# Kernel optimization log

Measured on AMD Instinct MI355X. Metric: run time of the kernel, lower is better.

Reference implementation:

```python
import jax, jax.numpy as jnp
import numpy as np

B, NQ, HW, D, H = 4, 100, 4096, 1024, 16
HD = D // H  # head dim = 64
EPS = 1e-5
NEG = -1e9


def layernorm(x, g, b):
    mu = jnp.mean(x, axis=-1, keepdims=True)
    var = jnp.mean(jnp.square(x - mu), axis=-1, keepdims=True)
    return (x - mu) * jax.lax.rsqrt(var + EPS) * g + b


def setup_inputs() -> dict:
    key = jax.random.key(0)
    ks = jax.random.split(key, 6)
    scale = 0.02
    return {
        "q": jax.random.normal(ks[0], (B, NQ, D), dtype=jnp.float32),
        "kv": jax.random.normal(ks[1], (B, HW, D), dtype=jnp.float32),
        "mask": jax.random.randint(ks[2], (B, NQ, HW), 0, 2, dtype=jnp.int32),
        "in_proj_w": scale * jax.random.normal(ks[3], (3 * D, D), dtype=jnp.float32),
        "in_proj_b": jnp.zeros((3 * D,), dtype=jnp.float32),
        "out_w": scale * jax.random.normal(ks[4], (D, D), dtype=jnp.float32),
        "out_b": jnp.zeros((D,), dtype=jnp.float32),
        "g_q": jnp.ones((D,), dtype=jnp.float32),
        "b_q": jnp.zeros((D,), dtype=jnp.float32),
        "g_kv": jnp.ones((D,), dtype=jnp.float32),
        "b_kv": jnp.zeros((D,), dtype=jnp.float32),
    }


def reference(q, kv, mask, in_proj_w, in_proj_b, out_w, out_b, g_q, b_q, g_kv, b_kv):
    qn = layernorm(q, g_q, b_q)      # [B,NQ,D]
    kvn = layernorm(kv, g_kv, b_kv)  # [B,HW,D]

    # nn.MultiheadAttention fused in-projection: rows [Wq; Wk; Wv]
    Wq, Wk, Wv = jnp.split(in_proj_w, 3, axis=0)
    bq, bk, bv = jnp.split(in_proj_b, 3, axis=0)
    qp = (qn @ Wq.T + bq).reshape(B, NQ, H, HD)
    kp = (kvn @ Wk.T + bk).reshape(B, HW, H, HD)
    vp = (kvn @ Wv.T + bv).reshape(B, HW, H, HD)

    scores = jnp.einsum("bqhd,bkhd->bhqk", qp, kp) / jnp.sqrt(jnp.float32(HD))

    # Per-query key mask; a query with an all-zero mask attends everywhere
    # (original code sets key_padding_mask=None when kpm.all()).
    allowed = mask.astype(bool)                                   # [B,NQ,HW]
    has_any = jnp.any(allowed, axis=-1, keepdims=True)
    eff = jnp.where(has_any, allowed, True)
    scores = jnp.where(eff[:, None, :, :], scores, NEG)

    attn = jax.nn.softmax(scores, axis=-1)                        # [B,H,NQ,HW]
    ctx = jnp.einsum("bhqk,bkhd->bqhd", attn, vp).reshape(B, NQ, D)
    return ctx @ out_w.T + out_b
```

## Files before the change

kernel.cpp:

```cpp
#include <hip/hip_runtime.h>
#include <math.h>
#include <stdint.h>

#define B_    4
#define NQ_   100
#define HW_   4096
#define D_    1024
#define H_    16
#define HD_   64
#define NCH_  8
#define KCH_  (HW_/NCH_)
#define QT_   32
#define MP_   512

typedef __attribute__((ext_vector_type(8))) short short8;
typedef __attribute__((ext_vector_type(8))) unsigned short ushort8v;
typedef __attribute__((ext_vector_type(4))) float f32x4;

__device__ __forceinline__ unsigned short f2bf(float f) {
    unsigned int u = __float_as_uint(f);
    u += 0x7fffu + ((u >> 16) & 1u);
    return (unsigned short)(u >> 16);
}
__device__ __forceinline__ float bf2f(unsigned short h) {
    return __uint_as_float(((unsigned int)h) << 16);
}

__device__ __forceinline__ void gl2lds16(const void* g, void* l) {
    typedef __attribute__((address_space(1))) unsigned int gu32;
    typedef __attribute__((address_space(3))) unsigned int lu32;
    __builtin_amdgcn_global_load_lds(
        reinterpret_cast<gu32*>(reinterpret_cast<uintptr_t>(g)),
        reinterpret_cast<lu32*>(reinterpret_cast<uintptr_t>(l)),
        16, 0, 0);
}

#define VMCNT3() asm volatile("s_waitcnt vmcnt(3)" ::: "memory")
#define VMCNT0() asm volatile("s_waitcnt vmcnt(0)" ::: "memory")
#define BARRIER() do { __builtin_amdgcn_s_barrier(); \
                       __builtin_amdgcn_sched_barrier(0); } while (0)

__global__ __launch_bounds__(256) void ln_bf16_kernel(
    const float* __restrict__ x, const float* __restrict__ g,
    const float* __restrict__ be, unsigned short* __restrict__ y, int real_rows)
{
    const int wv = threadIdx.x >> 6, lane = threadIdx.x & 63;
    const int row = blockIdx.x * 4 + wv;
    unsigned short* yr = y + (size_t)row * D_;
    if (row >= real_rows) {
        #pragma unroll
        for (int k = 0; k < 4; ++k)
            *reinterpret_cast<ushort4*>(yr + lane*4 + k*256) = make_ushort4(0,0,0,0);
        return;
    }
    const float* xr = x + (size_t)row * D_;
    float4 v[4];
    float s = 0.f, ss = 0.f;
    #pragma unroll
    for (int k = 0; k < 4; ++k) {
        v[k] = *reinterpret_cast<const float4*>(xr + lane*4 + k*256);
        s  += v[k].x + v[k].y + v[k].z + v[k].w;
        ss += v[k].x*v[k].x + v[k].y*v[k].y + v[k].z*v[k].z + v[k].w*v[k].w;
    }
    #pragma unroll
    for (int o = 1; o < 64; o <<= 1) {
        s  += __shfl_xor(s,  o);
        ss += __shfl_xor(ss, o);
    }
    const float mu = s * (1.0f / D_);
    const float rs = rsqrtf(ss * (1.0f / D_) - mu*mu + 1e-5f);
    #pragma unroll
    for (int k = 0; k < 4; ++k) {
        const float4 gg = *reinterpret_cast<const float4*>(g  + lane*4 + k*256);
        const float4 bb = *reinterpret_cast<const float4*>(be + lane*4 + k*256);
        ushort4 o;
        o.x = f2bf((v[k].x - mu) * rs * gg.x + bb.x);
        o.y = f2bf((v[k].y - mu) * rs * gg.y + bb.y);
        o.z = f2bf((v[k].z - mu) * rs * gg.z + bb.z);
        o.w = f2bf((v[k].w - mu) * rs * gg.w + bb.w);
        *reinterpret_cast<ushort4*>(yr + lane*4 + k*256) = o;
    }
}

__global__ __launch_bounds__(256) void wconv_kernel(
    const float* __restrict__ w, unsigned short* __restrict__ wb)
{
    const int i = blockIdx.x * 256 + threadIdx.x;
    const float4 v = reinterpret_cast<const float4*>(w)[i];
    ushort4 o;
    o.x = f2bf(v.x); o.y = f2bf(v.y); o.z = f2bf(v.z); o.w = f2bf(v.w);
    reinterpret_cast<ushort4*>(wb)[i] = o;
}

__global__ __launch_bounds__(256) void hilo_a_kernel(
    const float* __restrict__ x, unsigned short* __restrict__ y)
{
    const int row = blockIdx.x;
    const int tid = threadIdx.x;
    unsigned short* yr = y + (size_t)row * 3072;
    if (row >= B_*NQ_) {
        const ushort4 z = make_ushort4(0,0,0,0);
        reinterpret_cast<ushort4*>(yr)[tid]        = z;
        reinterpret_cast<ushort4*>(yr + 1024)[tid] = z;
        reinterpret_cast<ushort4*>(yr + 2048)[tid] = z;
        return;
    }
    const float4 v = reinterpret_cast<const float4*>(x + (size_t)row * D_)[tid];
    ushort4 hi, lo;
    hi.x = f2bf(v.x); hi.y = f2bf(v.y); hi.z = f2bf(v.z); hi.w = f2bf(v.w);
    lo.x = f2bf(v.x - bf2f(hi.x)); lo.y = f2bf(v.y - bf2f(hi.y));
    lo.z = f2bf(v.z - bf2f(hi.z)); lo.w = f2bf(v.w - bf2f(hi.w));
    reinterpret_cast<ushort4*>(yr)[tid]        = hi;
    reinterpret_cast<ushort4*>(yr + 1024)[tid] = lo;
    reinterpret_cast<ushort4*>(yr + 2048)[tid] = hi;
}

__global__ __launch_bounds__(256) void hilo_w_kernel(
    const float* __restrict__ w, unsigned short* __restrict__ y)
{
    const int row = blockIdx.x;
    const int tid = threadIdx.x;
    const float4 v = reinterpret_cast<const float4*>(w + (size_t)row * D_)[tid];
    ushort4 hi, lo;
    hi.x = f2bf(v.x); hi.y = f2bf(v.y); hi.z = f2bf(v.z); hi.w = f2bf(v.w);
    lo.x = f2bf(v.x - bf2f(hi.x)); lo.y = f2bf(v.y - bf2f(hi.y));
    lo.z = f2bf(v.z - bf2f(hi.z)); lo.w = f2bf(v.w - bf2f(hi.w));
    unsigned short* yr = y + (size_t)row * 3072;
    reinterpret_cast<ushort4*>(yr)[tid]        = hi;
    reinterpret_cast<ushort4*>(yr + 1024)[tid] = hi;
    reinterpret_cast<ushort4*>(yr + 2048)[tid] = lo;
}

__global__ __launch_bounds__(256) void mpack_kernel(
    const int* __restrict__ mask, unsigned int* __restrict__ mp)
{
    const int qrow = blockIdx.x;
    const int b = blockIdx.y;
    const int tid = threadIdx.x;
    unsigned int word = 0;
    if (qrow < NQ_ && tid < 128) {
        const int4* mr = reinterpret_cast<const int4*>(
            mask + ((size_t)(b*NQ_ + qrow))*HW_ + tid*32);
        #pragma unroll
        for (int j = 0; j < 8; ++j) {
            const int4 v = mr[j];
            word |= (v.x!=0 ? 1u:0u) << (4*j);
            word |= (v.y!=0 ? 1u:0u) << (4*j+1);
            word |= (v.z!=0 ? 1u:0u) << (4*j+2);
            word |= (v.w!=0 ? 1u:0u) << (4*j+3);
        }
    }
    const int wany = __any(word != 0) ? 1 : 0;
    __shared__ int red[4];
    if ((tid & 63) == 0) red[tid >> 6] = wany;
    __syncthreads();
    const int hasany = red[0] | red[1] | red[2] | red[3];
    if (tid < 128)
        mp[((size_t)(b*128 + qrow))*128 + tid] = hasany ? word : 0xFFFFFFFFu;
}

__global__ __launch_bounds__(512, 4) void gemm_kv_kernel(
    const unsigned short* __restrict__ A, const unsigned short* __restrict__ Wb,
    const float* __restrict__ bias, unsigned short* __restrict__ kp,
    unsigned short* __restrict__ vt)
{
    extern __shared__ __align__(16) unsigned short lds[];

    const int tid  = threadIdx.x;
    const int wave = tid >> 6;
    const int lane = tid & 63;
    const int lr   = lane & 15, quad = lane >> 4;
    const int wm2  = wave >> 2;
    const int wn4  = wave & 3;

    const int bn = blockIdx.x & 15;
    const int bm = blockIdx.x >> 4;

    const int srow = tid >> 2;
    const int sswz = (srow & 3) ^ ((srow >> 2) & 3);
    const int scol = ((tid & 3) ^ sswz) * 8;
    const unsigned short* aSrc0 = A  + (size_t)(bm*256 + srow      )*D_ + scol;
    const unsigned short* aSrc1 = A  + (size_t)(bm*256 + srow + 128)*D_ + scol;
    const unsigned short* bSrc  = Wb + (size_t)(bn*128 + srow      )*D_ + scol;
    const int wdst = wave * 512;

    int aoff[8], boff[2];
    #pragma unroll
    for (int fm = 0; fm < 8; ++fm) {
        const int row = wm2*128 + fm*16 + lr;
        aoff[fm] = row*32 + (quad ^ (row & 3) ^ ((row >> 2) & 3))*8;
    }
    #pragma unroll
    for (int fn = 0; fn < 2; ++fn) {
        const int row = wn4*32 + fn*16 + lr;
        boff[fn] = 8192 + row*32 + (quad ^ (row & 3) ^ ((row >> 2) & 3))*8;
    }

    f32x4 acc[8][2];
    #pragma unroll
    for (int i = 0; i < 8; ++i)
        #pragma unroll
        for (int j = 0; j < 2; ++j)
            acc[i][j] = (f32x4){0.f, 0.f, 0.f, 0.f};

    #pragma unroll
    for (int pt = 0; pt < 2; ++pt) {
        gl2lds16(aSrc0 + pt*32, lds + pt*12288 +        wdst);
        gl2lds16(aSrc1 + pt*32, lds + pt*12288 + 4096 + wdst);
        gl2lds16(bSrc  + pt*32, lds + pt*12288 + 8192 + wdst);
    }
    aSrc0 += 64; aSrc1 += 64; bSrc += 64;
    VMCNT3();
    BARRIER();

    int cur = 0, nx2 = 2;
    #pragma unroll 1
    for (int t = 0; t < 32; ++t) {
        const unsigned short* Sl = lds + cur*12288;
        unsigned short*       S2 = lds + nx2*12288;
        short8 afr[4], bfr[2];

        #pragma unroll
        for (int fm = 0; fm < 4; ++fm)
            afr[fm] = *reinterpret_cast<const short8*>(&Sl[aoff[fm]]);
        bfr[0] = *reinterpret_cast<const short8*>(&Sl[boff[0]]);
        bfr[1] = *reinterpret_cast<const short8*>(&Sl[boff[1]]);
        if (t < 30) {
            gl2lds16(aSrc0, S2 +        wdst);
            gl2lds16(aSrc1, S2 + 4096 + wdst);
        }
        __builtin_amdgcn_s_setprio(1);
        #pragma unroll
        for (int fm = 0; fm < 4; ++fm)
            #pragma unroll
            for (int fn = 0; fn < 2; ++fn)
                acc[fm][fn] = __builtin_amdgcn_mfma_f32_16x16x32_bf16(
                    afr[fm], bfr[fn], acc[fm][fn], 0, 0, 0);
        __builtin_amdgcn_s_setprio(0);

        #pragma unroll
        for (int fm = 0; fm < 4; ++fm)
            afr[fm] = *reinterpret_cast<const short8*>(&Sl[aoff[fm + 4]]);
        if (t < 30) {
            gl2lds16(bSrc, S2 + 8192 + wdst);
            aSrc0 += 32; aSrc1 += 32; bSrc += 32;
        }
        __builtin_amdgcn_s_setprio(1);
        #pragma unroll
        for (int fm = 0; fm < 4; ++fm)
            #pragma unroll
            for (int fn = 0; fn < 2; ++fn)
                acc[fm + 4][fn] = __builtin_amdgcn_mfma_f32_16x16x32_bf16(
                    afr[fm], bfr[fn], acc[fm + 4][fn], 0, 0, 0);
        __builtin_amdgcn_s_setprio(0);

        if (t < 30)       { VMCNT3(); }
        else if (t == 30) { VMCNT0(); }
        BARRIER();
        cur = (cur == 2) ? 0 : cur + 1;
        nx2 = (nx2 == 2) ? 0 : nx2 + 1;
    }

    const int colbase = bn*128 + wn4*32 + lr;
    const int mbase   = bm*256 + wm2*128 + quad*4;
    if (bn < 8) {
        #pragma unroll
        for (int fn = 0; fn < 2; ++fn) {
            const int n = colbase + fn*16;
            const float bb = bias[n];
            #pragma unroll
            for (int fm = 0; fm < 8; ++fm) {
                unsigned short* Cp = kp + (size_t)(mbase + fm*16)*1024 + n;
                #pragma unroll
                for (int r = 0; r < 4; ++r)
                    Cp[(size_t)r * 1024] = f2bf(acc[fm][fn][r] + bb);
            }
        }
    } else {
        const int b = bm >> 4;
        const int key0 = mbase - b*4096;
        #pragma unroll
        for (int fn = 0; fn < 2; ++fn) {
            const int n = colbase + fn*16;
            const float bb = bias[n];
            unsigned short* vrow = vt + (size_t)(b*1024 + n - 1024) * HW_;
            #pragma unroll
            for (int fm = 0; fm < 8; ++fm) {
                ushort4 o;
                o.x = f2bf(acc[fm][fn][0] + bb);
                o.y = f2bf(acc[fm][fn][1] + bb);
                o.z = f2bf(acc[fm][fn][2] + bb);
                o.w = f2bf(acc[fm][fn][3] + bb);
                *reinterpret_cast<ushort4*>(vrow + key0 + fm*16) = o;
            }
        }
    }
}

__global__ __launch_bounds__(256) void gemm_splitk_kernel(
    const unsigned short* __restrict__ A, const unsigned short* __restrict__ W,
    float* __restrict__ P, int K, int KS)
{
    __shared__ __align__(16) unsigned short As[2048];
    __shared__ __align__(16) unsigned short Bs[2048];
    const int tid = threadIdx.x;
    const int wave = tid >> 6, lane = tid & 63;
    const int lr = lane & 15, quad = lane >> 4;
    const int bn = blockIdx.x, bm = blockIdx.y, sk = blockIdx.z;

    const int r0 = tid >> 2;
    const int xs = (r0 & 3) ^ ((r0 >> 2) & 3);
    const int kc = (tid & 3) ^ xs;
    const unsigned short* ap = A + (size_t)(bm*64 + r0)*K + sk*KS + kc*8;
    const unsigned short* bp = W + (size_t)(bn*64 + r0)*K + sk*KS + kc*8;
    unsigned short* asd = As + wave*512;
    unsigned short* bsd = Bs + wave*512;

    f32x4 acc[4];
    #pragma unroll
    for (int j = 0; j < 4; ++j) acc[j] = (f32x4){0.f,0.f,0.f,0.f};

    const int arow = wave*16 + lr;
    const int xa = (arow & 3) ^ ((arow >> 2) & 3);
    const int aoff = (arow*4 + (quad ^ xa))*8;
    int boff[4];
    #pragma unroll
    for (int j = 0; j < 4; ++j) {
        const int brow = j*16 + lr;
        const int xb = (brow & 3) ^ ((brow >> 2) & 3);
        boff[j] = (brow*4 + (quad ^ xb))*8;
    }

    const int nsteps = KS >> 5;
    for (int s = 0; s < nsteps; ++s) {
        gl2lds16(ap, asd); gl2lds16(bp, bsd);
        ap += 32; bp += 32;
        __syncthreads();
        const short8 af = *reinterpret_cast<const short8*>(&As[aoff]);
        short8 bf[4];
        #pragma unroll
        for (int j = 0; j < 4; ++j)
            bf[j] = *reinterpret_cast<const short8*>(&Bs[boff[j]]);
        #pragma unroll
        for (int j = 0; j < 4; ++j)
            acc[j] = __builtin_amdgcn_mfma_f32_16x16x32_bf16(af, bf[j], acc[j], 0, 0, 0);
        __syncthreads();
    }

    float* Pb = P + ((size_t)sk*MP_ + bm*64)*1024 + bn*64;
    const int m0 = wave*16 + quad*4;
    #pragma unroll
    for (int j = 0; j < 4; ++j)
        #pragma unroll
        for (int r = 0; r < 4; ++r)
            Pb[(size_t)(m0 + r)*1024 + j*16 + lr] = acc[j][r];
}

__global__ __launch_bounds__(256) void reduce_kernel(
    const float* __restrict__ P, const float* __restrict__ bias,
    float* __restrict__ Cout, int SK)
{
    const int i4 = blockIdx.x * 256 + threadIdx.x;
    const int c4 = i4 & 255;
    float4 s = reinterpret_cast<const float4*>(bias)[c4];
    for (int sk = 0; sk < SK; ++sk) {
        const float4 p = reinterpret_cast<const float4*>(P + (size_t)sk*MP_*1024)[i4];
        s.x += p.x; s.y += p.y; s.z += p.z; s.w += p.w;
    }
    reinterpret_cast<float4*>(Cout)[i4] = s;
}

__global__ __launch_bounds__(256) void flash_kernel(
    const float* __restrict__ qp, const unsigned short* __restrict__ kp,
    const unsigned short* __restrict__ vt, const unsigned int* __restrict__ mpack,
    float* __restrict__ partO, float* __restrict__ partL)
{
    __shared__ __align__(16) unsigned char smem[49152];
    unsigned short* Ks  = (unsigned short*)smem;
    unsigned short* Vts = (unsigned short*)(smem + 16384);
    unsigned short* Qs  = (unsigned short*)(smem + 32768);
    unsigned short* Ps  = (unsigned short*)(smem + 37376);
    unsigned int*   MWs = (unsigned int*)  (smem + 47616);
    float*          mlW = (float*)         (smem + 48128);
    float*          Om  = (float*)smem;

    const int tid = threadIdx.x;
    const int wave = tid >> 6, lane = tid & 63;
    const int lr = lane & 15, quad = lane >> 4;
    const int qt = blockIdx.x, h = blockIdx.y;
    const int b = blockIdx.z >> 3, ks = blockIdx.z & 7;
    const int kb0 = ks * KCH_;

    {
        const int q = tid >> 3, dc = (tid & 7) * 8;
        const int qg = qt*QT_ + q;
        float4 v0 = make_float4(0.f,0.f,0.f,0.f), v1 = v0;
        if (qg < NQ_) {
            const float* src = qp + ((size_t)(b*NQ_ + qg))*D_ + h*HD_ + dc;
            v0 = *reinterpret_cast<const float4*>(src);
            v1 = *reinterpret_cast<const float4*>(src + 4);
        }
        ushort8v o;
        o[0]=f2bf(v0.x*0.125f); o[1]=f2bf(v0.y*0.125f);
        o[2]=f2bf(v0.z*0.125f); o[3]=f2bf(v0.w*0.125f);
        o[4]=f2bf(v1.x*0.125f); o[5]=f2bf(v1.y*0.125f);
        o[6]=f2bf(v1.z*0.125f); o[7]=f2bf(v1.w*0.125f);
        *reinterpret_cast<ushort8v*>(&Qs[q*72 + dc]) = o;
    }

    const unsigned short* kptr[4];
    const unsigned short* vptr[4];
    #pragma unroll
    for (int i = 0; i < 4; ++i) {
        const int s = i*256 + tid;
        const int key = s >> 3, jg = (s & 7) ^ (key & 7);
        kptr[i] = kp + ((size_t)(b*HW_) + kb0 + key)*1024 + h*HD_ + jg*8;
        const int d = s >> 4, js = s & 15, jg2 = js ^ (d & 15);
        vptr[i] = vt + ((size_t)(b*1024 + h*HD_ + d))*HW_ + kb0 + jg2*8;
    }

    int koff[2][2], voff[4];
    #pragma unroll
    for (int kj = 0; kj < 2; ++kj)
        #pragma unroll
        for (int ds = 0; ds < 2; ++ds) {
            const int key_l = wave*32 + kj*16 + lr;
            const int jg = ds*4 + quad;
            koff[kj][ds] = (key_l*8 + (jg ^ (key_l & 7))) * 8;
        }
    #pragma unroll
    for (int dj = 0; dj < 4; ++dj) {
        const int d_l = dj*16 + lr;
        const int jg = wave*4 + quad;
        voff[dj] = (d_l*16 + (jg ^ (d_l & 15))) * 8;
    }

    float lreg[8];
    #pragma unroll
    for (int i = 0; i < 8; ++i) lreg[i] = 0.f;
    f32x4 Ov[2][4];
    #pragma unroll
    for (int i = 0; i < 2; ++i)
        #pragma unroll
        for (int j = 0; j < 4; ++j)
            Ov[i][j] = (f32x4){0.f,0.f,0.f,0.f};

    for (int kt = 0; kt < 4; ++kt) {
        __syncthreads();
        #pragma unroll
        for (int i = 0; i < 4; ++i) {
            gl2lds16(kptr[i], Ks  + (i*256 + wave*64)*8);
            gl2lds16(vptr[i], Vts + (i*256 + wave*64)*8);
            kptr[i] += 128*1024; vptr[i] += 128;
        }
        if (tid < 128) {
            const int mw = tid >> 5, mq = tid & 31;
            MWs[mw*32 + mq] = mpack[((size_t)(b*128 + qt*QT_ + mq))*128 +
                                    (ks*16 + kt*4 + mw)];
        }
        __syncthreads();

        f32x4 S[2][2];
        #pragma unroll
        for (int i = 0; i < 2; ++i)
            #pragma unroll
            for (int kj = 0; kj < 2; ++kj)
                S[i][kj] = (f32x4){0.f,0.f,0.f,0.f};
        #pragma unroll
        for (int ds = 0; ds < 2; ++ds) {
            short8 aq[2], bk[2];
            aq[0] = *reinterpret_cast<const short8*>(&Qs[(     lr)*72 + ds*32 + quad*8]);
            aq[1] = *reinterpret_cast<const short8*>(&Qs[(16 + lr)*72 + ds*32 + quad*8]);
            bk[0] = *reinterpret_cast<const short8*>(&Ks[koff[0][ds]]);
            bk[1] = *reinterpret_cast<const short8*>(&Ks[koff[1][ds]]);
            #pragma unroll
            for (int i = 0; i < 2; ++i)
                #pragma unroll
                for (int kj = 0; kj < 2; ++kj)
                    S[i][kj] = __builtin_amdgcn_mfma_f32_16x16x32_bf16(
                        aq[i], bk[kj], S[i][kj], 0, 0, 0);
        }

        #pragma unroll
        for (int i = 0; i < 2; ++i) {
            #pragma unroll
            for (int r = 0; r < 4; ++r) {
                const int q = i*16 + quad*4 + r;
                const unsigned int mw = MWs[wave*32 + q];
                const float p0 = ((mw >> lr) & 1u)        ? __expf(S[i][0][r]) : 0.f;
                const float p1 = ((mw >> (16 + lr)) & 1u) ? __expf(S[i][1][r]) : 0.f;
                lreg[i*4+r] += p0 + p1;
                const float p0n = __shfl_xor(p0, 1);
                const float p1n = __shfl_xor(p1, 1);
                if (!(lr & 1)) {
                    const unsigned int w0 = (unsigned)f2bf(p0) | ((unsigned)f2bf(p0n) << 16);
                    const unsigned int w1 = (unsigned)f2bf(p1) | ((unsigned)f2bf(p1n) << 16);
                    *reinterpret_cast<unsigned int*>(&Ps[wave*1280 + q*40 + lr])      = w0;
                    *reinterpret_cast<unsigned int*>(&Ps[wave*1280 + q*40 + 16 + lr]) = w1;
                }
            }
        }

        short8 pf[2], vf[4];
        #pragma unroll
        for (int i = 0; i < 2; ++i)
            pf[i] = *reinterpret_cast<const short8*>(&Ps[wave*1280 + (i*16+lr)*40 + quad*8]);
        #pragma unroll
        for (int dj = 0; dj < 4; ++dj)
            vf[dj] = *reinterpret_cast<const short8*>(&Vts[voff[dj]]);
        #pragma unroll
        for (int i = 0; i < 2; ++i)
            #pragma unroll
            for (int dj = 0; dj < 4; ++dj)
                Ov[i][dj] = __builtin_amdgcn_mfma_f32_16x16x32_bf16(
                    pf[i], vf[dj], Ov[i][dj], 0, 0, 0);
    }

    __syncthreads();
    #pragma unroll
    for (int i = 0; i < 2; ++i)
        #pragma unroll
        for (int r = 0; r < 4; ++r) {
            float l = lreg[i*4+r];
            #pragma unroll
            for (int o = 1; o < 16; o <<= 1) l += __shfl_xor(l, o);
            if (lr == 0) mlW[wave*32 + i*16 + quad*4 + r] = l;
        }
    #pragma unroll
    for (int i = 0; i < 2; ++i)
        #pragma unroll
        for (int dj = 0; dj < 4; ++dj)
            #pragma unroll
            for (int r = 0; r < 4; ++r) {
                const int q = i*16 + quad*4 + r;
                Om[wave*2112 + q*66 + dj*16 + lr] = Ov[i][dj][r];
            }
    __syncthreads();
    {
        const int q = tid >> 3, dc = (tid & 7) * 8;
        float L = 0.f;
        #pragma unroll
        for (int w = 0; w < 4; ++w) L += mlW[w*32 + q];
        float os[8] = {};
        #pragma unroll
        for (int w = 0; w < 4; ++w)
            #pragma unroll
            for (int j = 0; j < 8; ++j)
                os[j] += Om[w*2112 + q*66 + dc + j];
        const size_t pr = (((size_t)(b*H_ + h))*NCH_ + ks)*128 + qt*QT_ + q;
        *reinterpret_cast<float4*>(&partO[pr*HD_ + dc])     = make_float4(os[0],os[1],os[2],os[3]);
        *reinterpret_cast<float4*>(&partO[pr*HD_ + dc + 4]) = make_float4(os[4],os[5],os[6],os[7]);
        if ((tid & 7) == 0) partL[pr] = L;
    }
}

__global__ __launch_bounds__(64) void combine_kernel(
    const float* __restrict__ partO, const float* __restrict__ partL,
    float* __restrict__ ctx)
{
    const int d = threadIdx.x;
    const int qi = blockIdx.x, h = blockIdx.y, b = blockIdx.z;
    const size_t base = ((size_t)(b*H_ + h)) * NCH_ * 128;
    float L = 0.f, O = 0.f;
    #pragma unroll
    for (int i = 0; i < NCH_; ++i) {
        const size_t r = base + i*128 + qi;
        L += partL[r];
        O += partO[r*HD_ + d];
    }
    ctx[((size_t)(b*NQ_ + qi))*D_ + h*HD_ + d] = O / L;
}

extern "C" void kernel_launch(void* const* d_in, const int* in_sizes, int n_in,
                              void* d_out, int out_size, void* d_ws, size_t ws_size,
                              hipStream_t stream)
{
    const float* q     = (const float*)d_in[0];
    const float* kv    = (const float*)d_in[1];
    const int*   mask  = (const int*)  d_in[2];
    const float* in_w  = (const float*)d_in[3];
    const float* in_b  = (const float*)d_in[4];
    const float* out_w = (const float*)d_in[5];
    const float* out_b = (const float*)d_in[6];
    const float* g_q   = (const float*)d_in[7];
    const float* b_q   = (const float*)d_in[8];
    const float* g_kv  = (const float*)d_in[9];
    const float* b_kv  = (const float*)d_in[10];
    float* out = (float*)d_out;

    char* ws = (char*)d_ws;
    float*          qp       = (float*)         (ws + 0);
    unsigned int*   mpackp   = (unsigned int*)  (ws + 1638400);
    unsigned short* wfull_bf = (unsigned short*)(ws + 1900544);
    unsigned short* qn_bf    = (unsigned short*)(ws + 8192000);
    unsigned short* ctx_cat  = (unsigned short*)(ws + 9240576);
    unsigned short* wout_cat = (unsigned short*)(ws + 12386304);
    float*          P        = (float*)         (ws + 18677760);
    float*          ctx      = (float*)         (ws + 35454976);
    float*          partL    = (float*)         (ws + 37093376);
    float*          partO    = (float*)         (ws + 37355520);
    unsigned short* kvn_bf   = (unsigned short*)(ws + 54132736);
    unsigned short* kp       = (unsigned short*)(ws + 87687168);
    unsigned short* vt       = (unsigned short*)(ws + 121241600);

    static bool attr_set = false;
    if (!attr_set) {
        hipFuncSetAttribute(reinterpret_cast<const void*>(gemm_kv_kernel),
                            hipFuncAttributeMaxDynamicSharedMemorySize, 73728);
        attr_set = true;
    }

    mpack_kernel<<<dim3(128, B_), 256, 0, stream>>>(mask, mpackp);
    wconv_kernel<<<3*D_*D_/4/256, 256, 0, stream>>>(in_w, wfull_bf);
    ln_bf16_kernel<<<B_*HW_/4, 256, 0, stream>>>(kv, g_kv, b_kv, kvn_bf, B_*HW_);
    ln_bf16_kernel<<<MP_/4, 256, 0, stream>>>(q, g_q, b_q, qn_bf, B_*NQ_);

    gemm_splitk_kernel<<<dim3(D_/64, MP_/64, 8), 256, 0, stream>>>(
        qn_bf, wfull_bf, P, D_, 128);
    reduce_kernel<<<B_*NQ_*D_/4/256, 256, 0, stream>>>(P, in_b, qp, 8);

    gemm_kv_kernel<<<dim3(1024), 512, 73728, stream>>>(
        kvn_bf, wfull_bf + (size_t)D_*D_, in_b + D_, kp, vt);

    flash_kernel<<<dim3(4, H_, B_*NCH_), 256, 0, stream>>>(
        qp, kp, vt, mpackp, partO, partL);
    combine_kernel<<<dim3(NQ_, H_, B_), 64, 0, stream>>>(partO, partL, ctx);

    hilo_a_kernel<<<MP_, 256, 0, stream>>>(ctx, ctx_cat);
    hilo_w_kernel<<<D_, 256, 0, stream>>>(out_w, wout_cat);
    gemm_splitk_kernel<<<dim3(D_/64, MP_/64, 8), 256, 0, stream>>>(
        ctx_cat, wout_cat, P, 3*D_, 384);
    reduce_kernel<<<B_*NQ_*D_/4/256, 256, 0, stream>>>(P, out_b, out, 8);
}
```

Before: 314.2 us.

## Reshape KV projection GEMM tile to 128x256 and remap block order

The KV projection GEMM tile changes from 256(M)x128(N) to 128(M)x256(N), so each wave now computes a 64x64 sub-tile with a 4x4 accumulator grid instead of 128x32. Fewer A-fragment LDS reads per MFMA improve register-level reuse. Block indices are remapped so the 8 consecutive blocks of a group share the same N slice across different M tiles, which aims to improve L2 reuse of the weight rows. The epilogue is adjusted to the new tile shape and the new batch index derivation. The risk is a different LDS bank pattern and changed write coalescing in the K/V stores.

```diff
diff --git a/kernel.cpp b/kernel.cpp
--- a/kernel.cpp
+++ b/kernel.cpp
@@ -173,43 +173,45 @@
     const int wm2  = wave >> 2;
     const int wn4  = wave & 3;
 
-    const int bn = blockIdx.x & 15;
-    const int bm = blockIdx.x >> 4;
+    const int x  = blockIdx.x & 7;
+    const int g  = blockIdx.x >> 3;
+    const int bm = x*16 + (g >> 3);
+    const int bn = g & 7;
 
     const int srow = tid >> 2;
     const int sswz = (srow & 3) ^ ((srow >> 2) & 3);
     const int scol = ((tid & 3) ^ sswz) * 8;
-    const unsigned short* aSrc0 = A  + (size_t)(bm*256 + srow      )*D_ + scol;
-    const unsigned short* aSrc1 = A  + (size_t)(bm*256 + srow + 128)*D_ + scol;
-    const unsigned short* bSrc  = Wb + (size_t)(bn*128 + srow      )*D_ + scol;
+    const unsigned short* aSrc  = A  + (size_t)(bm*128 + srow)*D_ + scol;
+    const unsigned short* bSrc0 = Wb + (size_t)(bn*256 + srow)*D_ + scol;
+    const unsigned short* bSrc1 = bSrc0 + (size_t)128*D_;
     const int wdst = wave * 512;
 
-    int aoff[8], boff[2];
-    #pragma unroll
-    for (int fm = 0; fm < 8; ++fm) {
-        const int row = wm2*128 + fm*16 + lr;
+    int aoff[4], boff[4];
+    #pragma unroll
+    for (int fm = 0; fm < 4; ++fm) {
+        const int row = wm2*64 + fm*16 + lr;
         aoff[fm] = row*32 + (quad ^ (row & 3) ^ ((row >> 2) & 3))*8;
     }
     #pragma unroll
-    for (int fn = 0; fn < 2; ++fn) {
-        const int row = wn4*32 + fn*16 + lr;
-        boff[fn] = 8192 + row*32 + (quad ^ (row & 3) ^ ((row >> 2) & 3))*8;
-    }
-
-    f32x4 acc[8][2];
-    #pragma unroll
-    for (int i = 0; i < 8; ++i)
-        #pragma unroll
-        for (int j = 0; j < 2; ++j)
+    for (int fn = 0; fn < 4; ++fn) {
+        const int row = wn4*64 + fn*16 + lr;
+        boff[fn] = 4096 + row*32 + (quad ^ (row & 3) ^ ((row >> 2) & 3))*8;
+    }
+
+    f32x4 acc[4][4];
+    #pragma unroll
+    for (int i = 0; i < 4; ++i)
+        #pragma unroll
+        for (int j = 0; j < 4; ++j)
             acc[i][j] = (f32x4){0.f, 0.f, 0.f, 0.f};
 
     #pragma unroll
     for (int pt = 0; pt < 2; ++pt) {
-        gl2lds16(aSrc0 + pt*32, lds + pt*12288 +        wdst);
-        gl2lds16(aSrc1 + pt*32, lds + pt*12288 + 4096 + wdst);
-        gl2lds16(bSrc  + pt*32, lds + pt*12288 + 8192 + wdst);
-    }
-    aSrc0 += 64; aSrc1 += 64; bSrc += 64;
+        gl2lds16(aSrc  + pt*32, lds + pt*12288 +        wdst);
+        gl2lds16(bSrc0 + pt*32, lds + pt*12288 + 4096 + wdst);
+        gl2lds16(bSrc1 + pt*32, lds + pt*12288 + 8192 + wdst);
+    }
+    aSrc += 64; bSrc0 += 64; bSrc1 += 64;
     VMCNT3();
     BARRIER();
 
@@ -218,7 +220,7 @@
     for (int t = 0; t < 32; ++t) {
         const unsigned short* Sl = lds + cur*12288;
         unsigned short*       S2 = lds + nx2*12288;
-        short8 afr[4], bfr[2];
+        short8 afr[4], bfr[4];
 
         #pragma unroll
         for (int fm = 0; fm < 4; ++fm)
@@ -226,8 +228,8 @@
         bfr[0] = *reinterpret_cast<const short8*>(&Sl[boff[0]]);
         bfr[1] = *reinterpret_cast<const short8*>(&Sl[boff[1]]);
         if (t < 30) {
-            gl2lds16(aSrc0, S2 +        wdst);
-            gl2lds16(aSrc1, S2 + 4096 + wdst);
+            gl2lds16(aSrc,  S2 +        wdst);
+            gl2lds16(bSrc0, S2 + 4096 + wdst);
         }
         __builtin_amdgcn_s_setprio(1);
         #pragma unroll
@@ -238,20 +240,19 @@
                     afr[fm], bfr[fn], acc[fm][fn], 0, 0, 0);
         __builtin_amdgcn_s_setprio(0);
 
+        bfr[2] = *reinterpret_cast<const short8*>(&Sl[boff[2]]);
+        bfr[3] = *reinterpret_cast<const short8*>(&Sl[boff[3]]);
+        if (t < 30) {
+            gl2lds16(bSrc1, S2 + 8192 + wdst);
+            aSrc += 32; bSrc0 += 32; bSrc1 += 32;
+        }
+        __builtin_amdgcn_s_setprio(1);
         #pragma unroll
         for (int fm = 0; fm < 4; ++fm)
-            afr[fm] = *reinterpret_cast<const short8*>(&Sl[aoff[fm + 4]]);
-        if (t < 30) {
-            gl2lds16(bSrc, S2 + 8192 + wdst);
-            aSrc0 += 32; aSrc1 += 32; bSrc += 32;
-        }
-        __builtin_amdgcn_s_setprio(1);
-        #pragma unroll
-        for (int fm = 0; fm < 4; ++fm)
-            #pragma unroll
-            for (int fn = 0; fn < 2; ++fn)
-                acc[fm + 4][fn] = __builtin_amdgcn_mfma_f32_16x16x32_bf16(
-                    afr[fm], bfr[fn], acc[fm + 4][fn], 0, 0, 0);
+            #pragma unroll
+            for (int fn = 2; fn < 4; ++fn)
+                acc[fm][fn] = __builtin_amdgcn_mfma_f32_16x16x32_bf16(
+                    afr[fm], bfr[fn], acc[fm][fn], 0, 0, 0);
         __builtin_amdgcn_s_setprio(0);
 
         if (t < 30)       { VMCNT3(); }
@@ -261,15 +262,15 @@
         nx2 = (nx2 == 2) ? 0 : nx2 + 1;
     }
 
-    const int colbase = bn*128 + wn4*32 + lr;
-    const int mbase   = bm*256 + wm2*128 + quad*4;
-    if (bn < 8) {
-        #pragma unroll
-        for (int fn = 0; fn < 2; ++fn) {
+    const int colbase = bn*256 + wn4*64 + lr;
+    const int mbase   = bm*128 + wm2*64 + quad*4;
+    if (bn < 4) {
+        #pragma unroll
+        for (int fn = 0; fn < 4; ++fn) {
             const int n = colbase + fn*16;
             const float bb = bias[n];
             #pragma unroll
-            for (int fm = 0; fm < 8; ++fm) {
+            for (int fm = 0; fm < 4; ++fm) {
                 unsigned short* Cp = kp + (size_t)(mbase + fm*16)*1024 + n;
                 #pragma unroll
                 for (int r = 0; r < 4; ++r)
@@ -277,15 +278,15 @@
             }
         }
     } else {
-        const int b = bm >> 4;
+        const int b = bm >> 5;
         const int key0 = mbase - b*4096;
         #pragma unroll
-        for (int fn = 0; fn < 2; ++fn) {
+        for (int fn = 0; fn < 4; ++fn) {
             const int n = colbase + fn*16;
             const float bb = bias[n];
             unsigned short* vrow = vt + (size_t)(b*1024 + n - 1024) * HW_;
             #pragma unroll
-            for (int fm = 0; fm < 8; ++fm) {
+            for (int fm = 0; fm < 4; ++fm) {
                 ushort4 o;
                 o.x = f2bf(acc[fm][fn][0] + bb);
                 o.y = f2bf(acc[fm][fn][1] + bb);
```

Result: no change. 313.3 us (-0.3%).
